# Optimization experiments

Measured on AMD Instinct MI355X. Metric: run time of the kernel, lower is better.

The kernel has to match this reference:

```python
import jax, jax.numpy as jnp
import numpy as np

N_HEADS = 8
EPS = 1e-5

def _mha(q_in, kv_in, wq, bq, wk, bk, wv, bv, wo, bo, causal):
    B, N, D = q_in.shape
    Dh = D // N_HEADS
    # projections (weights stored [in, out])
    Q = (q_in @ wq + bq).reshape(B, N, N_HEADS, Dh).swapaxes(1, 2)  # [B,H,N,Dh]
    K = (kv_in @ wk + bk).reshape(B, N, N_HEADS, Dh).swapaxes(1, 2)
    V = (kv_in @ wv + bv).reshape(B, N, N_HEADS, Dh).swapaxes(1, 2)
    scores = jnp.einsum('bhqd,bhkd->bhqk', Q, K) / jnp.sqrt(jnp.asarray(Dh, q_in.dtype))
    if causal:
        m = jnp.triu(jnp.ones((N, N), dtype=bool), k=1)
        scores = jnp.where(m, jnp.asarray(-jnp.inf, scores.dtype), scores)
    w = jax.nn.softmax(scores, axis=-1)
    attn = jnp.einsum('bhqk,bhkd->bhqd', w, V).swapaxes(1, 2).reshape(B, N, D)
    return attn @ wo + bo

def _ln(x, g, b):
    mu = jnp.mean(x, axis=-1, keepdims=True)
    var = jnp.var(x, axis=-1, keepdims=True)
    return (x - mu) / jnp.sqrt(var + EPS) * g + b

def setup_inputs() -> dict:
    key = jax.random.key(0)
    D, H, S = 512, 8, 4
    ks = jax.random.split(key, 32)
    def w(k, shape):
        return jax.random.normal(k, shape, dtype=jnp.float32) * 0.02
    inp = {
        'x': jax.random.normal(ks[0], (2, 2048, D), dtype=jnp.float32),
        'encoder_output': jax.random.normal(ks[1], (2, 2048, D), dtype=jnp.float32),
        # masked self-attention params
        'm_wq': w(ks[2], (D, D)), 'm_bq': jnp.zeros((D,), jnp.float32),
        'm_wk': w(ks[3], (D, D)), 'm_bk': jnp.zeros((D,), jnp.float32),
        'm_wv': w(ks[4], (D, D)), 'm_bv': jnp.zeros((D,), jnp.float32),
        'm_wo': w(ks[5], (D, D)), 'm_bo': jnp.zeros((D,), jnp.float32),
        # cross-attention params
        'c_wq': w(ks[6], (D, D)), 'c_bq': jnp.zeros((D,), jnp.float32),
        'c_wk': w(ks[7], (D, D)), 'c_bk': jnp.zeros((D,), jnp.float32),
        'c_wv': w(ks[8], (D, D)), 'c_bv': jnp.zeros((D,), jnp.float32),
        'c_wo': w(ks[9], (D, D)), 'c_bo': jnp.zeros((D,), jnp.float32),
        # layer norms
        'ln1_g': jnp.ones((D,), jnp.float32), 'ln1_b': jnp.zeros((D,), jnp.float32),
        'ln2_g': jnp.ones((D,), jnp.float32), 'ln2_b': jnp.zeros((D,), jnp.float32),
        'ln3_g': jnp.ones((D,), jnp.float32), 'ln3_b': jnp.zeros((D,), jnp.float32),
        # feed-forward (scale=4)
        'ff_w1': w(ks[10], (D, S * D)), 'ff_b1': jnp.zeros((S * D,), jnp.float32),
        'ff_w2': w(ks[11], (S * D, D)), 'ff_b2': jnp.zeros((D,), jnp.float32),
    }
    return inp

def reference(x, encoder_output,
              m_wq, m_bq, m_wk, m_bk, m_wv, m_bv, m_wo, m_bo,
              c_wq, c_bq, c_wk, c_bk, c_wv, c_bv, c_wo, c_bo,
              ln1_g, ln1_b, ln2_g, ln2_b, ln3_g, ln3_b,
              ff_w1, ff_b1, ff_w2, ff_b2):
    x = _mha(x, x, m_wq, m_bq, m_wk, m_bk, m_wv, m_bv, m_wo, m_bo, causal=True) + x
    x = _ln(x, ln1_g, ln1_b)
    x = _mha(x, encoder_output, c_wq, c_bq, c_wk, c_bk, c_wv, c_bv, c_wo, c_bo, causal=False) + x
    x = _ln(x, ln2_g, ln2_b)
    h = jax.nn.gelu(x @ ff_w1 + ff_b1, approximate=False)  # torch nn.GELU default = exact erf
    x = h @ ff_w2 + ff_b2 + x
    x = _ln(x, ln3_g, ln3_b)
    return x
```

## Files before the change

kernel.cpp:

```cpp
#include <hip/hip_runtime.h>
#include <hip/hip_bf16.h>

typedef __attribute__((ext_vector_type(8))) short short8;
typedef __attribute__((ext_vector_type(4))) float floatx4;
typedef unsigned short u16;
typedef unsigned int u32;

#define QSCALE 0.1803368801111244f

__device__ __forceinline__ u16 f2b(float f) {
    union { float f; u32 u; } v; v.f = f;
    u32 r = v.u + 0x7fffu + ((v.u >> 16) & 1u);
    return (u16)(r >> 16);
}

__device__ __forceinline__ float b2f(u16 b) {
    u32 u = ((u32)b) << 16;
    union { u32 u; float f; } v; v.u = u;
    return v.f;
}

__device__ __forceinline__ u32 pk2(float a, float b) {
    __hip_bfloat162 w = __float22bfloat162_rn(make_float2(a, b));
    return *(u32*)&w;
}

__device__ __forceinline__ void gload(const u16* g, u16* l) {
    __builtin_amdgcn_global_load_lds((const __attribute__((address_space(1))) void*)g,
                                     (__attribute__((address_space(3))) void*)l, 16, 0, 0);
}

struct TPent { const float* s; u16* d; int O; int dI; };
struct TP16 { TPent e[16]; };
__global__ __launch_bounds__(256) void transpose_convert16(TP16 p) {
    __shared__ float t[32][33];
    TPent e = p.e[blockIdx.z];
    int o0 = blockIdx.x * 32, i0 = blockIdx.y * 32;
    int tx = threadIdx.x, ty = threadIdx.y;
#pragma unroll
    for (int k = 0; k < 32; k += 8) t[ty + k][tx] = e.s[(size_t)(i0 + ty + k) * e.O + o0 + tx];
    __syncthreads();
#pragma unroll
    for (int k = 0; k < 32; k += 8) e.d[(size_t)(o0 + ty + k) * e.dI + i0 + tx] = f2b(t[tx][ty + k]);
}

__global__ __launch_bounds__(256) void gather_bias(const float* b0, const float* b1, const float* b2,
                                                   const float* b3, const float* b4,
                                                   float* dqkv, float* dkv) {
    int i = blockIdx.x * 256 + threadIdx.x;
    if      (i < 512)  dqkv[i] = b0[i];
    else if (i < 1024) dqkv[i] = b1[i - 512];
    else if (i < 1536) dqkv[i] = b2[i - 1024];
    else if (i < 2048) dkv[i - 1536] = b3[i - 1536];
    else               dkv[i - 1536] = b4[i - 2048];
}

__global__ __launch_bounds__(256) void cvt_bf16_2(const float4* __restrict__ s0, ushort4* __restrict__ d0,
                                                  const float4* __restrict__ s1, ushort4* __restrict__ d1) {
    int i = blockIdx.x * 256 + threadIdx.x;
    float4 v = s0[i];
    ushort4 o; o.x = f2b(v.x); o.y = f2b(v.y); o.z = f2b(v.z); o.w = f2b(v.w);
    d0[i] = o;
    v = s1[i];
    o.x = f2b(v.x); o.y = f2b(v.y); o.z = f2b(v.z); o.w = f2b(v.w);
    d1[i] = o;
}

__global__ __launch_bounds__(256) void gemm64x128(
    const u16* __restrict__ A, int lda,
    const u16* __restrict__ B, int ldb,
    int K,
    const float* __restrict__ bias,
    const float* __restrict__ residual,
    float* __restrict__ out_f, u16* __restrict__ out_b,
    int out_stride, int scale_ncols, int gelu_flag)
{
    __shared__ u16 lA[64 * 64];
    __shared__ u16 lB[128 * 64];
    int tid = threadIdx.x, wave = tid >> 6, lane = tid & 63;
    int g4 = lane >> 4, c16 = lane & 15;
    int swz = (c16 & 7) << 3;
    int bm = blockIdx.x * 64, bn = blockIdx.y * 128;
    int wm = (wave >> 1) * 32, wn = (wave & 1) * 64;
    int srow = tid >> 3, skseg = ((tid & 7) * 8) ^ ((srow & 7) << 3);
    const u16* Ar = A + (size_t)(bm + srow) * lda + skseg;
    const u16* Br = B + (size_t)(bn + srow) * ldb + skseg;
    size_t a32 = (size_t)32 * lda, b32 = (size_t)32 * ldb;

    floatx4 acc[2][4];
#pragma unroll
    for (int i = 0; i < 2; i++)
#pragma unroll
        for (int j = 0; j < 4; j++) acc[i][j] = (floatx4){0.f, 0.f, 0.f, 0.f};

    for (int kt = 0; kt < K; kt += 64) {
        __syncthreads();
        gload(Ar + kt,           lA + wave * 512);
        gload(Ar + kt + a32,     lA + 2048 + wave * 512);
        gload(Br + kt,           lB + wave * 512);
        gload(Br + kt + b32,     lB + 2048 + wave * 512);
        gload(Br + kt + 2 * b32, lB + 4096 + wave * 512);
        gload(Br + kt + 3 * b32, lB + 6144 + wave * 512);
        __syncthreads();
        short8 aF[2][2], bF[2][4];
#pragma unroll
        for (int kk = 0; kk < 2; kk++) {
            int ko = (g4 * 8 + kk * 32) ^ swz;
#pragma unroll
            for (int i = 0; i < 2; i++) aF[kk][i] = *(const short8*)&lA[(wm + i * 16 + c16) * 64 + ko];
#pragma unroll
            for (int j = 0; j < 4; j++) bF[kk][j] = *(const short8*)&lB[(wn + j * 16 + c16) * 64 + ko];
        }
#pragma unroll
        for (int kk = 0; kk < 2; kk++)
#pragma unroll
            for (int i = 0; i < 2; i++)
#pragma unroll
                for (int j = 0; j < 4; j++)
                    acc[i][j] = __builtin_amdgcn_mfma_f32_16x16x32_bf16(aF[kk][i], bF[kk][j], acc[i][j], 0, 0, 0);
    }

#pragma unroll
    for (int i = 0; i < 2; i++) {
        int row0 = bm + wm + i * 16 + g4 * 4;
#pragma unroll
        for (int j = 0; j < 4; j++) {
            int col = bn + wn + j * 16 + c16;
            float bv = bias[col];
#pragma unroll
            for (int r = 0; r < 4; r++) {
                int row = row0 + r;
                float v = acc[i][j][r] + bv;
                if (col < scale_ncols) v *= QSCALE;
                if (gelu_flag) v = 0.5f * v * (1.f + erff(v * 0.70710678118654752f));
                if (residual) v += residual[(size_t)row * out_stride + col];
                if (out_f) out_f[(size_t)row * out_stride + col] = v;
                else       out_b[(size_t)row * out_stride + col] = f2b(v);
            }
        }
    }
}

__global__ __launch_bounds__(256) void gemm64x128_dual(
    const u16* __restrict__ A0, const u16* __restrict__ B0, const float* __restrict__ bias0,
    u16* __restrict__ out0, int ostride0, int scale0,
    const u16* __restrict__ A1, const u16* __restrict__ B1, const float* __restrict__ bias1,
    u16* __restrict__ out1, int ostride1,
    int ys, int K, int lda, int ldb)
{
    __shared__ u16 lA[64 * 64];
    __shared__ u16 lB[128 * 64];
    int tid = threadIdx.x, wave = tid >> 6, lane = tid & 63;
    int g4 = lane >> 4, c16 = lane & 15;
    int swz = (c16 & 7) << 3;
    int by = blockIdx.y;
    const u16* A; const u16* B; const float* bias; u16* out; int ostride, scaleN, bn;
    if (by < ys) { A = A0; B = B0; bias = bias0; out = out0; ostride = ostride0; scaleN = scale0; bn = by * 128; }
    else         { A = A1; B = B1; bias = bias1; out = out1; ostride = ostride1; scaleN = 0;      bn = (by - ys) * 128; }
    int bm = blockIdx.x * 64;
    int wm = (wave >> 1) * 32, wn = (wave & 1) * 64;
    int srow = tid >> 3, skseg = ((tid & 7) * 8) ^ ((srow & 7) << 3);
    const u16* Ar = A + (size_t)(bm + srow) * lda + skseg;
    const u16* Br = B + (size_t)(bn + srow) * ldb + skseg;
    size_t a32 = (size_t)32 * lda, b32 = (size_t)32 * ldb;

    floatx4 acc[2][4];
#pragma unroll
    for (int i = 0; i < 2; i++)
#pragma unroll
        for (int j = 0; j < 4; j++) acc[i][j] = (floatx4){0.f, 0.f, 0.f, 0.f};

    for (int kt = 0; kt < K; kt += 64) {
        __syncthreads();
        gload(Ar + kt,           lA + wave * 512);
        gload(Ar + kt + a32,     lA + 2048 + wave * 512);
        gload(Br + kt,           lB + wave * 512);
        gload(Br + kt + b32,     lB + 2048 + wave * 512);
        gload(Br + kt + 2 * b32, lB + 4096 + wave * 512);
        gload(Br + kt + 3 * b32, lB + 6144 + wave * 512);
        __syncthreads();
        short8 aF[2][2], bF[2][4];
#pragma unroll
        for (int kk = 0; kk < 2; kk++) {
            int ko = (g4 * 8 + kk * 32) ^ swz;
#pragma unroll
            for (int i = 0; i < 2; i++) aF[kk][i] = *(const short8*)&lA[(wm + i * 16 + c16) * 64 + ko];
#pragma unroll
            for (int j = 0; j < 4; j++) bF[kk][j] = *(const short8*)&lB[(wn + j * 16 + c16) * 64 + ko];
        }
#pragma unroll
        for (int kk = 0; kk < 2; kk++)
#pragma unroll
            for (int i = 0; i < 2; i++)
#pragma unroll
                for (int j = 0; j < 4; j++)
                    acc[i][j] = __builtin_amdgcn_mfma_f32_16x16x32_bf16(aF[kk][i], bF[kk][j], acc[i][j], 0, 0, 0);
    }

#pragma unroll
    for (int i = 0; i < 2; i++) {
        int row0 = bm + wm + i * 16 + g4 * 4;
#pragma unroll
        for (int j = 0; j < 4; j++) {
            int col = bn + wn + j * 16 + c16;
            float bv = bias[col];
#pragma unroll
            for (int r = 0; r < 4; r++) {
                float v = acc[i][j][r] + bv;
                if (col < scaleN) v *= QSCALE;
                out[(size_t)(row0 + r) * ostride + col] = f2b(v);
            }
        }
    }
}

__global__ __launch_bounds__(256) void gemm64x64(
    const u16* __restrict__ A, int lda,
    const u16* __restrict__ B, int ldb,
    int K,
    const float* __restrict__ bias,
    u16* __restrict__ out_b,
    int out_stride, int scale_ncols)
{
    __shared__ u16 lA[64 * 64];
    __shared__ u16 lB[64 * 64];
    int tid = threadIdx.x, wave = tid >> 6, lane = tid & 63;
    int g4 = lane >> 4, c16 = lane & 15;
    int swz = (c16 & 7) << 3;
    int bm = blockIdx.x * 64, bn = blockIdx.y * 64;
    int wm = wave * 16;
    int srow = tid >> 3, skseg = ((tid & 7) * 8) ^ ((srow & 7) << 3);
    const u16* Ar = A + (size_t)(bm + srow) * lda + skseg;
    const u16* Br = B + (size_t)(bn + srow) * ldb + skseg;
    size_t a32 = (size_t)32 * lda, b32 = (size_t)32 * ldb;

    floatx4 acc[4];
#pragma unroll
    for (int j = 0; j < 4; j++) acc[j] = (floatx4){0.f, 0.f, 0.f, 0.f};

    for (int kt = 0; kt < K; kt += 64) {
        __syncthreads();
        gload(Ar + kt,       lA + wave * 512);
        gload(Ar + kt + a32, lA + 2048 + wave * 512);
        gload(Br + kt,       lB + wave * 512);
        gload(Br + kt + b32, lB + 2048 + wave * 512);
        __syncthreads();
        short8 aF[2], bF[2][4];
#pragma unroll
        for (int kk = 0; kk < 2; kk++) {
            int ko = (g4 * 8 + kk * 32) ^ swz;
            aF[kk] = *(const short8*)&lA[(wm + c16) * 64 + ko];
#pragma unroll
            for (int j = 0; j < 4; j++) bF[kk][j] = *(const short8*)&lB[(j * 16 + c16) * 64 + ko];
        }
#pragma unroll
        for (int kk = 0; kk < 2; kk++)
#pragma unroll
            for (int j = 0; j < 4; j++)
                acc[j] = __builtin_amdgcn_mfma_f32_16x16x32_bf16(aF[kk], bF[kk][j], acc[j], 0, 0, 0);
    }

    int row0 = bm + wm + g4 * 4;
#pragma unroll
    for (int j = 0; j < 4; j++) {
        int col = bn + j * 16 + c16;
        float bv = bias[col];
#pragma unroll
        for (int r = 0; r < 4; r++) {
            int row = row0 + r;
            float v = acc[j][r] + bv;
            if (col < scale_ncols) v *= QSCALE;
            out_b[(size_t)row * out_stride + col] = f2b(v);
        }
    }
}

__global__ __launch_bounds__(256) void gemm64x64s(
    const u16* __restrict__ A, int lda,
    const u16* __restrict__ B, int ldb,
    int Ksub,
    const float* __restrict__ bias,
    const float* __restrict__ res_f,
    const u16* __restrict__ res_b,
    u16* __restrict__ out0, int out_stride)
{
    __shared__ u16 lA[64 * 64];
    __shared__ u16 lB[64 * 64];
    int tid = threadIdx.x, wave = tid >> 6, lane = tid & 63;
    int g4 = lane >> 4, c16 = lane & 15;
    int swz = (c16 & 7) << 3;
    int bm = blockIdx.x * 64, bn = blockIdx.y * 64, sp = blockIdx.z;
    int wm = wave * 16;
    int srow = tid >> 3;
    int skseg = (((tid & 7) * 8) ^ ((srow & 7) << 3)) + sp * Ksub;
    const u16* Ar = A + (size_t)(bm + srow) * lda + skseg;
    const u16* Br = B + (size_t)(bn + srow) * ldb + skseg;
    size_t a32 = (size_t)32 * lda, b32 = (size_t)32 * ldb;

    floatx4 acc[4];
#pragma unroll
    for (int j = 0; j < 4; j++) acc[j] = (floatx4){0.f, 0.f, 0.f, 0.f};

    for (int kt = 0; kt < Ksub; kt += 64) {
        __syncthreads();
        gload(Ar + kt,       lA + wave * 512);
        gload(Ar + kt + a32, lA + 2048 + wave * 512);
        gload(Br + kt,       lB + wave * 512);
        gload(Br + kt + b32, lB + 2048 + wave * 512);
        __syncthreads();
        short8 aF[2], bF[2][4];
#pragma unroll
        for (int kk = 0; kk < 2; kk++) {
            int ko = (g4 * 8 + kk * 32) ^ swz;
            aF[kk] = *(const short8*)&lA[(wm + c16) * 64 + ko];
#pragma unroll
            for (int j = 0; j < 4; j++) bF[kk][j] = *(const short8*)&lB[(j * 16 + c16) * 64 + ko];
        }
#pragma unroll
        for (int kk = 0; kk < 2; kk++)
#pragma unroll
            for (int j = 0; j < 4; j++)
                acc[j] = __builtin_amdgcn_mfma_f32_16x16x32_bf16(aF[kk], bF[kk][j], acc[j], 0, 0, 0);
    }

    u16* out = out0 + (size_t)sp * 4096 * 512;
    int row0 = bm + wm + g4 * 4;
#pragma unroll
    for (int j = 0; j < 4; j++) {
        int col = bn + j * 16 + c16;
        float bv = (sp == 0) ? bias[col] : 0.f;
#pragma unroll
        for (int r = 0; r < 4; r++) {
            int row = row0 + r;
            float v = acc[j][r] + bv;
            if (sp == 0) {
                if (res_f)      v += res_f[(size_t)row * out_stride + col];
                else if (res_b) v += b2f(res_b[(size_t)row * out_stride + col]);
            }
            out[(size_t)row * out_stride + col] = f2b(v);
        }
    }
}

__global__ __launch_bounds__(256, 4) void attn_causal_paired(
    const u16* __restrict__ Qp, int q_stride,
    const u16* __restrict__ Kp, int kv_stride,
    const u16* __restrict__ Vp,
    u16* __restrict__ Opart,
    float* __restrict__ Lpart)
{
    __shared__ u16 lK[64 * 72];
    __shared__ u16 lVT[64 * 72];
    int tid = threadIdx.x, wave = tid >> 6, lane = tid & 63;
    int g4 = lane >> 4, c16 = lane & 15;
    int id = blockIdx.x;
    int bh = (id & 7) | ((id >> 3 & 1) << 3);
    int rest = id >> 4;
    int p = rest & 15;
    int sp = rest >> 4;
    int qtA = p, qtB = 31 - p;
    size_t rowbase = (size_t)(bh >> 3) * 2048;
    int hoff = (bh & 7) * 64;
    const u16* Q = Qp + rowbase * q_stride + hoff;
    const u16* K = Kp + rowbase * kv_stride + hoff;
    const u16* V = Vp + rowbase * kv_stride + hoff;

    int qrowA = qtA * 64 + wave * 16;
    int qrowB = qtB * 64 + wave * 16;
    short8 qa0 = *(const short8*)&Q[(size_t)(qrowA + c16) * q_stride + g4 * 8];
    short8 qa1 = *(const short8*)&Q[(size_t)(qrowA + c16) * q_stride + g4 * 8 + 32];
    short8 qb0 = *(const short8*)&Q[(size_t)(qrowB + c16) * q_stride + g4 * 8];
    short8 qb1 = *(const short8*)&Q[(size_t)(qrowB + c16) * q_stride + g4 * 8 + 32];

    int kr = tid >> 2, ks = (tid & 3) * 16;
    int krow = 16 * (2 * (kr >> 5) + ((kr >> 2) & 1)) + 4 * ((kr >> 3) & 3) + (kr & 3);
    const u16* Kbase = K + (size_t)kr * kv_stride + ks;
    int vk0 = (tid >> 3) * 2, vs = (tid & 7) * 8;
    const u16* Vbase = V + (size_t)vk0 * kv_stride + vs;

    int4 kv0, kv1, vv0, vv1;
    auto load_tile = [&](int kt) {
        const u16* kp = Kbase + (size_t)kt * 64 * kv_stride;
        kv0 = *(const int4*)(kp);
        kv1 = *(const int4*)(kp + 8);
        const u16* vp = Vbase + (size_t)kt * 64 * kv_stride;
        vv0 = *(const int4*)(vp);
        vv1 = *(const int4*)(vp + kv_stride);
    };
    auto store_tile = [&]() {
        *(int4*)&lK[krow * 72 + ks] = kv0;
        *(int4*)&lK[krow * 72 + ks + 8] = kv1;
        const u16* pa = (const u16*)&vv0;
        const u16* pb = (const u16*)&vv1;
#pragma unroll
        for (int j = 0; j < 8; j++) {
            int dh = vs + j;
            int keyS = vk0 ^ (((dh >> 3) & 3) << 4);
            u32 w = (u32)pa[j] | ((u32)pb[j] << 16);
            *(u32*)&lVT[dh * 72 + keyS] = w;
        }
    };

    floatx4 oA[4], oB[4];
#pragma unroll
    for (int d = 0; d < 4; d++) { oA[d] = (floatx4){0.f,0.f,0.f,0.f}; oB[d] = (floatx4){0.f,0.f,0.f,0.f}; }
    float lsA = 0.f, lsB = 0.f;

    auto compute_tile = [&](short8 qf0, short8 qf1, floatx4 (&oacc)[4], float& lsum,
                            bool diag, int qtile, int kt) {
        floatx4 sc[4];
#pragma unroll
        for (int nt = 0; nt < 4; nt++) {
            short8 b0 = *(const short8*)&lK[(nt * 16 + c16) * 72 + g4 * 8];
            short8 b1 = *(const short8*)&lK[(nt * 16 + c16) * 72 + g4 * 8 + 32];
            floatx4 z = (floatx4){0.f, 0.f, 0.f, 0.f};
            z = __builtin_amdgcn_mfma_f32_16x16x32_bf16(b0, qf0, z, 0, 0, 0);
            z = __builtin_amdgcn_mfma_f32_16x16x32_bf16(b1, qf1, z, 0, 0, 0);
            sc[nt] = z;
        }
        if (diag) {
            int qr = qtile * 64 + wave * 16 + c16;
#pragma unroll
            for (int nt = 0; nt < 4; nt++) {
                int key0 = kt * 64 + 8 * g4 + 4 * (nt & 1) + 32 * (nt >> 1);
#pragma unroll
                for (int r = 0; r < 4; r++)
                    if (key0 + r > qr) sc[nt][r] = -1e30f;
            }
        }
        float e[4][4];
#pragma unroll
        for (int nt = 0; nt < 4; nt++)
#pragma unroll
            for (int r = 0; r < 4; r++) e[nt][r] = exp2f(sc[nt][r]);
        float s0 = (e[0][0] + e[0][1]) + (e[0][2] + e[0][3]);
        float s1 = (e[1][0] + e[1][1]) + (e[1][2] + e[1][3]);
        float s2 = (e[2][0] + e[2][1]) + (e[2][2] + e[2][3]);
        float s3 = (e[3][0] + e[3][1]) + (e[3][2] + e[3][3]);
        lsum += (s0 + s1) + (s2 + s3);
        short8 pa0, pa1;
        {
            u32 w[8];
            w[0] = pk2(e[0][0], e[0][1]); w[1] = pk2(e[0][2], e[0][3]);
            w[2] = pk2(e[1][0], e[1][1]); w[3] = pk2(e[1][2], e[1][3]);
            w[4] = pk2(e[2][0], e[2][1]); w[5] = pk2(e[2][2], e[2][3]);
            w[6] = pk2(e[3][0], e[3][1]); w[7] = pk2(e[3][2], e[3][3]);
            pa0 = *(short8*)&w[0];
            pa1 = *(short8*)&w[4];
        }
#pragma unroll
        for (int d = 0; d < 4; d++) {
            int vswz = ((2 * d + (c16 >> 3)) & 3) << 4;
            short8 vb0 = *(const short8*)&lVT[(d * 16 + c16) * 72 + ((g4 * 8) ^ vswz)];
            short8 vb1 = *(const short8*)&lVT[(d * 16 + c16) * 72 + ((32 + g4 * 8) ^ vswz)];
            oacc[d] = __builtin_amdgcn_mfma_f32_16x16x32_bf16(pa0, vb0, oacc[d], 0, 0, 0);
            oacc[d] = __builtin_amdgcn_mfma_f32_16x16x32_bf16(pa1, vb1, oacc[d], 0, 0, 0);
        }
    };

    int t = sp;
    load_tile(t <= p ? t : t - p - 1);
    for (; t < 33; t += 4) {
        __syncthreads();
        store_tile();
        __syncthreads();
        if (t + 4 < 33) { int tn = t + 4; load_tile(tn <= p ? tn : tn - p - 1); }
        if (t <= p) compute_tile(qa0, qa1, oA, lsA, t == p,  qtA, t);
        else        compute_tile(qb0, qb1, oB, lsB, t == 32, qtB, t - p - 1);
    }

    lsA += __shfl_xor(lsA, 16); lsA += __shfl_xor(lsA, 32);
    lsB += __shfl_xor(lsB, 16); lsB += __shfl_xor(lsB, 32);
    size_t slab = (size_t)(sp * 16 + bh) * 2048;
    if (g4 == 0) {
        Lpart[slab + qrowA + c16] = lsA;
        Lpart[slab + qrowB + c16] = lsB;
    }
    u16* ObA = Opart + (slab + qrowA) * 64;
    u16* ObB = Opart + (slab + qrowB) * 64;
#pragma unroll
    for (int d = 0; d < 4; d++)
#pragma unroll
        for (int r = 0; r < 4; r++) {
            ObA[(size_t)(4 * g4 + r) * 64 + d * 16 + c16] = f2b(oA[d][r]);
            ObB[(size_t)(4 * g4 + r) * 64 + d * 16 + c16] = f2b(oB[d][r]);
        }
}

__global__ __launch_bounds__(256) void attn_fused(
    const u16* __restrict__ Qp, int q_stride,
    const u16* __restrict__ Kp, int kv_stride,
    const u16* __restrict__ Vp,
    u16* __restrict__ Opart,
    float* __restrict__ Lpart)
{
    __shared__ u16 lK[64 * 72];
    __shared__ u16 lVT[64 * 72];
    int tid = threadIdx.x, wave = tid >> 6, lane = tid & 63;
    int g4 = lane >> 4, c16 = lane & 15;
    int id = blockIdx.x;
    int bh = (id & 7) | ((id >> 3 & 1) << 3);
    int rest = id >> 4;
    int qt = rest & 31;
    int sp = rest >> 5;
    size_t rowbase = (size_t)(bh >> 3) * 2048;
    int hoff = (bh & 7) * 64;
    const u16* Q = Qp + rowbase * q_stride + hoff;
    const u16* K = Kp + rowbase * kv_stride + hoff;
    const u16* V = Vp + rowbase * kv_stride + hoff;

    int qrow0 = qt * 64 + wave * 16;
    short8 qf0 = *(const short8*)&Q[(size_t)(qrow0 + c16) * q_stride + g4 * 8];
    short8 qf1 = *(const short8*)&Q[(size_t)(qrow0 + c16) * q_stride + g4 * 8 + 32];

    int kr = tid >> 2, ks = (tid & 3) * 16;
    int krow = 16 * (2 * (kr >> 5) + ((kr >> 2) & 1)) + 4 * ((kr >> 3) & 3) + (kr & 3);
    const u16* Kbase = K + (size_t)kr * kv_stride + ks;
    int vk0 = (tid >> 3) * 2, vs = (tid & 7) * 8;
    const u16* Vbase = V + (size_t)vk0 * kv_stride + vs;

    int4 kv0, kv1, vv0, vv1;
    auto load_tile = [&](int kt) {
        const u16* kp = Kbase + (size_t)kt * 64 * kv_stride;
        kv0 = *(const int4*)(kp);
        kv1 = *(const int4*)(kp + 8);
        const u16* vp = Vbase + (size_t)kt * 64 * kv_stride;
        vv0 = *(const int4*)(vp);
        vv1 = *(const int4*)(vp + kv_stride);
    };
    auto store_tile = [&]() {
        *(int4*)&lK[krow * 72 + ks] = kv0;
        *(int4*)&lK[krow * 72 + ks + 8] = kv1;
        const u16* pa = (const u16*)&vv0;
        const u16* pb = (const u16*)&vv1;
#pragma unroll
        for (int j = 0; j < 8; j++) {
            int dh = vs + j;
            int keyS = vk0 ^ (((dh >> 3) & 3) << 4);
            u32 w = (u32)pa[j] | ((u32)pb[j] << 16);
            *(u32*)&lVT[dh * 72 + keyS] = w;
        }
    };

    floatx4 o_acc[4];
#pragma unroll
    for (int d = 0; d < 4; d++) o_acc[d] = (floatx4){0.f, 0.f, 0.f, 0.f};
    float lsum = 0.f;

    int kt = sp;
    load_tile(kt);
    for (; kt < 32; kt += 4) {
        __syncthreads();
        store_tile();
        __syncthreads();
        if (kt + 4 < 32) load_tile(kt + 4);

        floatx4 sc[4];
#pragma unroll
        for (int nt = 0; nt < 4; nt++) {
            short8 b0 = *(const short8*)&lK[(nt * 16 + c16) * 72 + g4 * 8];
            short8 b1 = *(const short8*)&lK[(nt * 16 + c16) * 72 + g4 * 8 + 32];
            floatx4 z = (floatx4){0.f, 0.f, 0.f, 0.f};
            z = __builtin_amdgcn_mfma_f32_16x16x32_bf16(b0, qf0, z, 0, 0, 0);
            z = __builtin_amdgcn_mfma_f32_16x16x32_bf16(b1, qf1, z, 0, 0, 0);
            sc[nt] = z;
        }
        float e[4][4];
#pragma unroll
        for (int nt = 0; nt < 4; nt++)
#pragma unroll
            for (int r = 0; r < 4; r++) e[nt][r] = exp2f(sc[nt][r]);
        float s0 = (e[0][0] + e[0][1]) + (e[0][2] + e[0][3]);
        float s1 = (e[1][0] + e[1][1]) + (e[1][2] + e[1][3]);
        float s2 = (e[2][0] + e[2][1]) + (e[2][2] + e[2][3]);
        float s3 = (e[3][0] + e[3][1]) + (e[3][2] + e[3][3]);
        lsum += (s0 + s1) + (s2 + s3);
        short8 pa0, pa1;
        {
            u32 w[8];
            w[0] = pk2(e[0][0], e[0][1]); w[1] = pk2(e[0][2], e[0][3]);
            w[2] = pk2(e[1][0], e[1][1]); w[3] = pk2(e[1][2], e[1][3]);
            w[4] = pk2(e[2][0], e[2][1]); w[5] = pk2(e[2][2], e[2][3]);
            w[6] = pk2(e[3][0], e[3][1]); w[7] = pk2(e[3][2], e[3][3]);
            pa0 = *(short8*)&w[0];
            pa1 = *(short8*)&w[4];
        }
#pragma unroll
        for (int d = 0; d < 4; d++) {
            int swz = ((2 * d + (c16 >> 3)) & 3) << 4;
            short8 vb0 = *(const short8*)&lVT[(d * 16 + c16) * 72 + ((g4 * 8) ^ swz)];
            short8 vb1 = *(const short8*)&lVT[(d * 16 + c16) * 72 + ((32 + g4 * 8) ^ swz)];
            o_acc[d] = __builtin_amdgcn_mfma_f32_16x16x32_bf16(pa0, vb0, o_acc[d], 0, 0, 0);
            o_acc[d] = __builtin_amdgcn_mfma_f32_16x16x32_bf16(pa1, vb1, o_acc[d], 0, 0, 0);
        }
    }

    lsum += __shfl_xor(lsum, 16);
    lsum += __shfl_xor(lsum, 32);
    size_t slab = (size_t)(sp * 16 + bh) * 2048;
    if (g4 == 0) Lpart[slab + qrow0 + c16] = lsum;
    u16* Ob = Opart + (slab + qrow0) * 64;
#pragma unroll
    for (int d = 0; d < 4; d++)
#pragma unroll
        for (int r = 0; r < 4; r++)
            Ob[(size_t)(4 * g4 + r) * 64 + d * 16 + c16] = f2b(o_acc[d][r]);
}

__global__ __launch_bounds__(256) void attn_combine(
    const ushort4* __restrict__ Op,
    const float* __restrict__ Lp,
    ushort4* __restrict__ out)
{
    int e = blockIdx.x * 256 + threadIdx.x;
    int dh4 = e & 15;
    int qrow = (e >> 4) & 2047;
    int bh = e >> 15;
    int li = bh * 2048 + qrow;
    float l = (Lp[li] + Lp[32768 + li]) + (Lp[65536 + li] + Lp[98304 + li]);
    float inv = 1.f / l;
    ushort4 a = Op[e];
    ushort4 b = Op[524288 + e];
    ushort4 c = Op[2 * 524288 + e];
    ushort4 d = Op[3 * 524288 + e];
    ushort4 o;
    o.x = f2b(((b2f(a.x) + b2f(b.x)) + (b2f(c.x) + b2f(d.x))) * inv);
    o.y = f2b(((b2f(a.y) + b2f(b.y)) + (b2f(c.y) + b2f(d.y))) * inv);
    o.z = f2b(((b2f(a.z) + b2f(b.z)) + (b2f(c.z) + b2f(d.z))) * inv);
    o.w = f2b(((b2f(a.w) + b2f(b.w)) + (b2f(c.w) + b2f(d.w))) * inv);
    int row = (bh >> 3) * 2048 + qrow;
    out[(size_t)row * 128 + (bh & 7) * 16 + dh4] = o;
}

__global__ __launch_bounds__(256) void ln_kernel(const u16* __restrict__ in0,
                                                 const u16* __restrict__ in1,
                                                 const float* __restrict__ g,
                                                 const float* __restrict__ b,
                                                 float* __restrict__ out_f,
                                                 u16* __restrict__ out_b)
{
    const int D = 512;
    int row = blockIdx.x, tid = threadIdx.x;
    size_t base = (size_t)row * D;
    float v0 = b2f(in0[base + tid]) + b2f(in1[base + tid]);
    float v1 = b2f(in0[base + tid + 256]) + b2f(in1[base + tid + 256]);
    float s = v0 + v1, ss = v0 * v0 + v1 * v1;
#pragma unroll
    for (int off = 1; off < 64; off <<= 1) { s += __shfl_xor(s, off); ss += __shfl_xor(ss, off); }
    __shared__ float red[8];
    int wave = tid >> 6, lane = tid & 63;
    if (lane == 0) { red[wave] = s; red[4 + wave] = ss; }
    __syncthreads();
    float st = red[0] + red[1] + red[2] + red[3];
    float sst = red[4] + red[5] + red[6] + red[7];
    float mu = st * (1.f / 512.f);
    float var = sst * (1.f / 512.f) - mu * mu;
    float rs = rsqrtf(var + 1e-5f);
    float y0 = (v0 - mu) * rs * g[tid] + b[tid];
    float y1 = (v1 - mu) * rs * g[tid + 256] + b[tid + 256];
    if (out_f) { out_f[base + tid] = y0; out_f[base + tid + 256] = y1; }
    if (out_b) { out_b[base + tid] = f2b(y0); out_b[base + tid + 256] = f2b(y1); }
}

extern "C" void kernel_launch(void* const* d_in, const int* in_sizes, int n_in,
                              void* d_out, int out_size, void* d_ws, size_t ws_size,
                              hipStream_t stream)
{
    (void)in_sizes; (void)n_in; (void)out_size; (void)ws_size;
    const float* x     = (const float*)d_in[0];
    const float* enc   = (const float*)d_in[1];
    const float* m_wq  = (const float*)d_in[2];  const float* m_bq = (const float*)d_in[3];
    const float* m_wk  = (const float*)d_in[4];  const float* m_bk = (const float*)d_in[5];
    const float* m_wv  = (const float*)d_in[6];  const float* m_bv = (const float*)d_in[7];
    const float* m_wo  = (const float*)d_in[8];  const float* m_bo = (const float*)d_in[9];
    const float* c_wq  = (const float*)d_in[10]; const float* c_bq = (const float*)d_in[11];
    const float* c_wk  = (const float*)d_in[12]; const float* c_bk = (const float*)d_in[13];
    const float* c_wv  = (const float*)d_in[14]; const float* c_bv = (const float*)d_in[15];
    const float* c_wo  = (const float*)d_in[16]; const float* c_bo = (const float*)d_in[17];
    const float* ln1_g = (const float*)d_in[18]; const float* ln1_b = (const float*)d_in[19];
    const float* ln2_g = (const float*)d_in[20]; const float* ln2_b = (const float*)d_in[21];
    const float* ln3_g = (const float*)d_in[22]; const float* ln3_b = (const float*)d_in[23];
    const float* ff_w1 = (const float*)d_in[24]; const float* ff_b1 = (const float*)d_in[25];
    const float* ff_w2 = (const float*)d_in[26]; const float* ff_b2 = (const float*)d_in[27];

    char* base = (char*)d_ws; size_t off = 0;
    auto alloc = [&](size_t bytes) -> void* {
        void* p = base + off; off = (off + bytes + 255) & ~(size_t)255; return p;
    };
    u16*   Wqkv_m = (u16*)alloc(1536 * 512 * 2);
    u16*   Wo_m   = (u16*)alloc(512 * 512 * 2);
    u16*   Wq_c   = (u16*)alloc(512 * 512 * 2);
    u16*   Wkv_c  = (u16*)alloc(1024 * 512 * 2);
    u16*   Wo_c   = (u16*)alloc(512 * 512 * 2);
    u16*   W1t    = (u16*)alloc(2048 * 512 * 2);
    u16*   W2t    = (u16*)alloc(512 * 2048 * 2);
    float* bqkv_m = (float*)alloc(1536 * 4);
    float* bkv_c  = (float*)alloc(1024 * 4);
    u16*   xb     = (u16*)alloc((size_t)4096 * 512 * 2);
    u16*   encb   = (u16*)alloc((size_t)4096 * 512 * 2);
    u16*   qkvm   = (u16*)alloc((size_t)4096 * 1536 * 2);
    u16*   attnm  = (u16*)alloc((size_t)4096 * 512 * 2);
    u16*   y01    = (u16*)alloc((size_t)2 * 4096 * 512 * 2);
    u16*   x1b    = (u16*)alloc((size_t)4096 * 512 * 2);
    u16*   qc     = (u16*)alloc((size_t)4096 * 512 * 2);
    u16*   kvc    = (u16*)alloc((size_t)4096 * 1024 * 2);
    u16*   attnc  = (u16*)alloc((size_t)4096 * 512 * 2);
    u16*   x2b    = (u16*)alloc((size_t)4096 * 512 * 2);
    u16*   h      = (u16*)alloc((size_t)4096 * 2048 * 2);
    u16*   Opart  = (u16*)alloc((size_t)4 * 16 * 2048 * 64 * 2);
    float* Lpart  = (float*)alloc((size_t)4 * 16 * 2048 * 4);

    TP16 tp;
    tp.e[0] = {m_wq, Wqkv_m,              512, 512};
    tp.e[1] = {m_wk, Wqkv_m + 512 * 512,  512, 512};
    tp.e[2] = {m_wv, Wqkv_m + 1024 * 512, 512, 512};
    tp.e[3] = {m_wo, Wo_m,                512, 512};
    tp.e[4] = {c_wq, Wq_c,                512, 512};
    tp.e[5] = {c_wk, Wkv_c,               512, 512};
    tp.e[6] = {c_wv, Wkv_c + 512 * 512,   512, 512};
    tp.e[7] = {c_wo, Wo_c,                512, 512};
    for (int k = 0; k < 4; k++)
        tp.e[8 + k]  = {ff_w1 + 512 * k,        W1t + k * 512 * 512, 2048, 512};
    for (int k = 0; k < 4; k++)
        tp.e[12 + k] = {ff_w2 + (size_t)512 * k * 512, W2t + 512 * k, 512, 2048};
    transpose_convert16<<<dim3(16, 16, 16), dim3(32, 8), 0, stream>>>(tp);
    gather_bias<<<10, 256, 0, stream>>>(m_bq, m_bk, m_bv, c_bk, c_bv, bqkv_m, bkv_c);
    cvt_bf16_2<<<2048, 256, 0, stream>>>((const float4*)x, (ushort4*)xb,
                                         (const float4*)enc, (ushort4*)encb);

    gemm64x128_dual<<<dim3(64, 20), 256, 0, stream>>>(
        xb, Wqkv_m, bqkv_m, qkvm, 1536, 512,
        encb, Wkv_c, bkv_c, kvc, 1024,
        12, 512, 512, 512);

    attn_causal_paired<<<1024, 256, 0, stream>>>(qkvm, 1536, qkvm + 512, 1536, qkvm + 1024,
                                                 Opart, Lpart);
    attn_combine<<<2048, 256, 0, stream>>>((const ushort4*)Opart, Lpart, (ushort4*)attnm);
    gemm64x64s<<<dim3(64, 8, 2), 256, 0, stream>>>(attnm, 512, Wo_m, 512, 256,
                                                   m_bo, x, nullptr, y01, 512);
    ln_kernel<<<4096, 256, 0, stream>>>(y01, y01 + (size_t)4096 * 512, ln1_g, ln1_b,
                                        nullptr, x1b);

    gemm64x64<<<dim3(64, 8), 256, 0, stream>>>(x1b, 512, Wq_c, 512, 512,
                                               c_bq, qc, 512, 512);
    attn_fused<<<2048, 256, 0, stream>>>(qc, 512, kvc, 1024, kvc + 512,
                                         Opart, Lpart);
    attn_combine<<<2048, 256, 0, stream>>>((const ushort4*)Opart, Lpart, (ushort4*)attnc);
    gemm64x64s<<<dim3(64, 8, 2), 256, 0, stream>>>(attnc, 512, Wo_c, 512, 256,
                                                   c_bo, nullptr, x1b, y01, 512);
    ln_kernel<<<4096, 256, 0, stream>>>(y01, y01 + (size_t)4096 * 512, ln2_g, ln2_b,
                                        nullptr, x2b);

    gemm64x128<<<dim3(64, 16), 256, 0, stream>>>(x2b, 512, W1t, 512, 512,
                                                 ff_b1, nullptr, nullptr, h, 2048, 0, 1);
    gemm64x64s<<<dim3(64, 8, 2), 256, 0, stream>>>(h, 2048, W2t, 2048, 1024,
                                                   ff_b2, nullptr, x2b, y01, 512);
    ln_kernel<<<4096, 256, 0, stream>>>(y01, y01 + (size_t)4096 * 512, ln3_g, ln3_b,
                                        (float*)d_out, nullptr);
}
```

Before: 308.0 us.

## Use 128-row query tiles per block in causal and cross attention

Both attention kernels now give each wave 32 query rows (two 16-row MFMA chunks) instead of 16. Every K/V tile staged in LDS therefore feeds twice as many query rows, and the grids shrink to 512 and 1024 blocks. The causal kernel keeps its paired light/heavy scheduling, rescaled to 128-row tiles over 34 key steps split four ways, with masking applied on the diagonal tiles. The cost is more registers per thread (occupancy hints lowered to 2 and 3 blocks) and fewer blocks to spread across the CUs.

```diff
diff --git a/kernel.cpp b/kernel.cpp
--- a/kernel.cpp
+++ b/kernel.cpp
@@ -342,7 +342,8 @@
     }
 }
 
-__global__ __launch_bounds__(256, 4) void attn_causal_paired(
+
+__global__ __launch_bounds__(256, 3) void attn_cross(
     const u16* __restrict__ Qp, int q_stride,
     const u16* __restrict__ Kp, int kv_stride,
     const u16* __restrict__ Vp,
@@ -356,21 +357,21 @@
     int id = blockIdx.x;
     int bh = (id & 7) | ((id >> 3 & 1) << 3);
     int rest = id >> 4;
-    int p = rest & 15;
+    int qt = rest & 15;
     int sp = rest >> 4;
-    int qtA = p, qtB = 31 - p;
     size_t rowbase = (size_t)(bh >> 3) * 2048;
     int hoff = (bh & 7) * 64;
     const u16* Q = Qp + rowbase * q_stride + hoff;
     const u16* K = Kp + rowbase * kv_stride + hoff;
     const u16* V = Vp + rowbase * kv_stride + hoff;
 
-    int qrowA = qtA * 64 + wave * 16;
-    int qrowB = qtB * 64 + wave * 16;
-    short8 qa0 = *(const short8*)&Q[(size_t)(qrowA + c16) * q_stride + g4 * 8];
-    short8 qa1 = *(const short8*)&Q[(size_t)(qrowA + c16) * q_stride + g4 * 8 + 32];
-    short8 qb0 = *(const short8*)&Q[(size_t)(qrowB + c16) * q_stride + g4 * 8];
-    short8 qb1 = *(const short8*)&Q[(size_t)(qrowB + c16) * q_stride + g4 * 8 + 32];
+    int qbase = qt * 128 + wave * 32;
+    short8 qf[2][2];
+#pragma unroll
+    for (int qc = 0; qc < 2; qc++) {
+        qf[qc][0] = *(const short8*)&Q[(size_t)(qbase + qc * 16 + c16) * q_stride + g4 * 8];
+        qf[qc][1] = *(const short8*)&Q[(size_t)(qbase + qc * 16 + c16) * q_stride + g4 * 8 + 32];
+    }
 
     int kr = tid >> 2, ks = (tid & 3) * 16;
     int krow = 16 * (2 * (kr >> 5) + ((kr >> 2) & 1)) + 4 * ((kr >> 3) & 3) + (kr & 3);
@@ -401,93 +402,88 @@
         }
     };
 
-    floatx4 oA[4], oB[4];
-#pragma unroll
-    for (int d = 0; d < 4; d++) { oA[d] = (floatx4){0.f,0.f,0.f,0.f}; oB[d] = (floatx4){0.f,0.f,0.f,0.f}; }
-    float lsA = 0.f, lsB = 0.f;
-
-    auto compute_tile = [&](short8 qf0, short8 qf1, floatx4 (&oacc)[4], float& lsum,
-                            bool diag, int qtile, int kt) {
-        floatx4 sc[4];
+    floatx4 o[2][4];
+#pragma unroll
+    for (int qc = 0; qc < 2; qc++)
+#pragma unroll
+        for (int d = 0; d < 4; d++) o[qc][d] = (floatx4){0.f, 0.f, 0.f, 0.f};
+    float ls0 = 0.f, ls1 = 0.f;
+
+    int kt = sp;
+    load_tile(kt);
+    for (; kt < 32; kt += 4) {
+        __syncthreads();
+        store_tile();
+        __syncthreads();
+        if (kt + 4 < 32) load_tile(kt + 4);
+
+        short8 b0[4], b1[4];
 #pragma unroll
         for (int nt = 0; nt < 4; nt++) {
-            short8 b0 = *(const short8*)&lK[(nt * 16 + c16) * 72 + g4 * 8];
-            short8 b1 = *(const short8*)&lK[(nt * 16 + c16) * 72 + g4 * 8 + 32];
-            floatx4 z = (floatx4){0.f, 0.f, 0.f, 0.f};
-            z = __builtin_amdgcn_mfma_f32_16x16x32_bf16(b0, qf0, z, 0, 0, 0);
-            z = __builtin_amdgcn_mfma_f32_16x16x32_bf16(b1, qf1, z, 0, 0, 0);
-            sc[nt] = z;
-        }
-        if (diag) {
-            int qr = qtile * 64 + wave * 16 + c16;
+            b0[nt] = *(const short8*)&lK[(nt * 16 + c16) * 72 + g4 * 8];
+            b1[nt] = *(const short8*)&lK[(nt * 16 + c16) * 72 + g4 * 8 + 32];
+        }
+        short8 pa[2][2];
+#pragma unroll
+        for (int qc = 0; qc < 2; qc++) {
+            floatx4 sc[4];
 #pragma unroll
             for (int nt = 0; nt < 4; nt++) {
-                int key0 = kt * 64 + 8 * g4 + 4 * (nt & 1) + 32 * (nt >> 1);
-#pragma unroll
-                for (int r = 0; r < 4; r++)
-                    if (key0 + r > qr) sc[nt][r] = -1e30f;
+                floatx4 z = (floatx4){0.f, 0.f, 0.f, 0.f};
+                z = __builtin_amdgcn_mfma_f32_16x16x32_bf16(b0[nt], qf[qc][0], z, 0, 0, 0);
+                z = __builtin_amdgcn_mfma_f32_16x16x32_bf16(b1[nt], qf[qc][1], z, 0, 0, 0);
+                sc[nt] = z;
             }
-        }
-        float e[4][4];
-#pragma unroll
-        for (int nt = 0; nt < 4; nt++)
-#pragma unroll
-            for (int r = 0; r < 4; r++) e[nt][r] = exp2f(sc[nt][r]);
-        float s0 = (e[0][0] + e[0][1]) + (e[0][2] + e[0][3]);
-        float s1 = (e[1][0] + e[1][1]) + (e[1][2] + e[1][3]);
-        float s2 = (e[2][0] + e[2][1]) + (e[2][2] + e[2][3]);
-        float s3 = (e[3][0] + e[3][1]) + (e[3][2] + e[3][3]);
-        lsum += (s0 + s1) + (s2 + s3);
-        short8 pa0, pa1;
-        {
+            float e[4][4];
+#pragma unroll
+            for (int nt = 0; nt < 4; nt++)
+#pragma unroll
+                for (int r = 0; r < 4; r++) e[nt][r] = exp2f(sc[nt][r]);
+            float s0 = (e[0][0] + e[0][1]) + (e[0][2] + e[0][3]);
+            float s1 = (e[1][0] + e[1][1]) + (e[1][2] + e[1][3]);
+            float s2 = (e[2][0] + e[2][1]) + (e[2][2] + e[2][3]);
+            float s3 = (e[3][0] + e[3][1]) + (e[3][2] + e[3][3]);
+            if (qc == 0) ls0 += (s0 + s1) + (s2 + s3);
+            else         ls1 += (s0 + s1) + (s2 + s3);
             u32 w[8];
             w[0] = pk2(e[0][0], e[0][1]); w[1] = pk2(e[0][2], e[0][3]);
             w[2] = pk2(e[1][0], e[1][1]); w[3] = pk2(e[1][2], e[1][3]);
             w[4] = pk2(e[2][0], e[2][1]); w[5] = pk2(e[2][2], e[2][3]);
             w[6] = pk2(e[3][0], e[3][1]); w[7] = pk2(e[3][2], e[3][3]);
-            pa0 = *(short8*)&w[0];
-            pa1 = *(short8*)&w[4];
+            pa[qc][0] = *(short8*)&w[0];
+            pa[qc][1] = *(short8*)&w[4];
         }
 #pragma unroll
         for (int d = 0; d < 4; d++) {
             int vswz = ((2 * d + (c16 >> 3)) & 3) << 4;
             short8 vb0 = *(const short8*)&lVT[(d * 16 + c16) * 72 + ((g4 * 8) ^ vswz)];
             short8 vb1 = *(const short8*)&lVT[(d * 16 + c16) * 72 + ((32 + g4 * 8) ^ vswz)];
-            oacc[d] = __builtin_amdgcn_mfma_f32_16x16x32_bf16(pa0, vb0, oacc[d], 0, 0, 0);
-            oacc[d] = __builtin_amdgcn_mfma_f32_16x16x32_bf16(pa1, vb1, oacc[d], 0, 0, 0);
-        }
-    };
-
-    int t = sp;
-    load_tile(t <= p ? t : t - p - 1);
-    for (; t < 33; t += 4) {
-        __syncthreads();
-        store_tile();
-        __syncthreads();
-        if (t + 4 < 33) { int tn = t + 4; load_tile(tn <= p ? tn : tn - p - 1); }
-        if (t <= p) compute_tile(qa0, qa1, oA, lsA, t == p,  qtA, t);
-        else        compute_tile(qb0, qb1, oB, lsB, t == 32, qtB, t - p - 1);
-    }
-
-    lsA += __shfl_xor(lsA, 16); lsA += __shfl_xor(lsA, 32);
-    lsB += __shfl_xor(lsB, 16); lsB += __shfl_xor(lsB, 32);
+            o[0][d] = __builtin_amdgcn_mfma_f32_16x16x32_bf16(pa[0][0], vb0, o[0][d], 0, 0, 0);
+            o[0][d] = __builtin_amdgcn_mfma_f32_16x16x32_bf16(pa[0][1], vb1, o[0][d], 0, 0, 0);
+            o[1][d] = __builtin_amdgcn_mfma_f32_16x16x32_bf16(pa[1][0], vb0, o[1][d], 0, 0, 0);
+            o[1][d] = __builtin_amdgcn_mfma_f32_16x16x32_bf16(pa[1][1], vb1, o[1][d], 0, 0, 0);
+        }
+    }
+
+    ls0 += __shfl_xor(ls0, 16); ls0 += __shfl_xor(ls0, 32);
+    ls1 += __shfl_xor(ls1, 16); ls1 += __shfl_xor(ls1, 32);
     size_t slab = (size_t)(sp * 16 + bh) * 2048;
     if (g4 == 0) {
-        Lpart[slab + qrowA + c16] = lsA;
-        Lpart[slab + qrowB + c16] = lsB;
-    }
-    u16* ObA = Opart + (slab + qrowA) * 64;
-    u16* ObB = Opart + (slab + qrowB) * 64;
-#pragma unroll
-    for (int d = 0; d < 4; d++)
-#pragma unroll
-        for (int r = 0; r < 4; r++) {
-            ObA[(size_t)(4 * g4 + r) * 64 + d * 16 + c16] = f2b(oA[d][r]);
-            ObB[(size_t)(4 * g4 + r) * 64 + d * 16 + c16] = f2b(oB[d][r]);
-        }
-}
-
-__global__ __launch_bounds__(256) void attn_fused(
+        Lpart[slab + qbase + c16] = ls0;
+        Lpart[slab + qbase + 16 + c16] = ls1;
+    }
+#pragma unroll
+    for (int qc = 0; qc < 2; qc++) {
+        u16* Ob = Opart + (slab + qbase + qc * 16) * 64;
+#pragma unroll
+        for (int d = 0; d < 4; d++)
+#pragma unroll
+            for (int r = 0; r < 4; r++)
+                Ob[(size_t)(4 * g4 + r) * 64 + d * 16 + c16] = f2b(o[qc][d][r]);
+    }
+}
+
+__global__ __launch_bounds__(256, 2) void attn_causal_paired(
     const u16* __restrict__ Qp, int q_stride,
     const u16* __restrict__ Kp, int kv_stride,
     const u16* __restrict__ Vp,
@@ -501,17 +497,26 @@
     int id = blockIdx.x;
     int bh = (id & 7) | ((id >> 3 & 1) << 3);
     int rest = id >> 4;
-    int qt = rest & 31;
-    int sp = rest >> 5;
+    int p = rest & 7;
+    int sp = rest >> 3;
+    int TqA = p, TqB = 15 - p;
+    int splitA = 2 * p + 2;
     size_t rowbase = (size_t)(bh >> 3) * 2048;
     int hoff = (bh & 7) * 64;
     const u16* Q = Qp + rowbase * q_stride + hoff;
     const u16* K = Kp + rowbase * kv_stride + hoff;
     const u16* V = Vp + rowbase * kv_stride + hoff;
 
-    int qrow0 = qt * 64 + wave * 16;
-    short8 qf0 = *(const short8*)&Q[(size_t)(qrow0 + c16) * q_stride + g4 * 8];
-    short8 qf1 = *(const short8*)&Q[(size_t)(qrow0 + c16) * q_stride + g4 * 8 + 32];
+    int qbA = TqA * 128 + wave * 32;
+    int qbB = TqB * 128 + wave * 32;
+    short8 qfA[2][2], qfB[2][2];
+#pragma unroll
+    for (int qc = 0; qc < 2; qc++) {
+        qfA[qc][0] = *(const short8*)&Q[(size_t)(qbA + qc * 16 + c16) * q_stride + g4 * 8];
+        qfA[qc][1] = *(const short8*)&Q[(size_t)(qbA + qc * 16 + c16) * q_stride + g4 * 8 + 32];
+        qfB[qc][0] = *(const short8*)&Q[(size_t)(qbB + qc * 16 + c16) * q_stride + g4 * 8];
+        qfB[qc][1] = *(const short8*)&Q[(size_t)(qbB + qc * 16 + c16) * q_stride + g4 * 8 + 32];
+    }
 
     int kr = tid >> 2, ks = (tid & 3) * 16;
     int krow = 16 * (2 * (kr >> 5) + ((kr >> 2) & 1)) + 4 * ((kr >> 3) & 3) + (kr & 3);
@@ -531,80 +536,124 @@
     auto store_tile = [&]() {
         *(int4*)&lK[krow * 72 + ks] = kv0;
         *(int4*)&lK[krow * 72 + ks + 8] = kv1;
-        const u16* pa = (const u16*)&vv0;
-        const u16* pb = (const u16*)&vv1;
+        const u16* pa_ = (const u16*)&vv0;
+        const u16* pb_ = (const u16*)&vv1;
 #pragma unroll
         for (int j = 0; j < 8; j++) {
             int dh = vs + j;
             int keyS = vk0 ^ (((dh >> 3) & 3) << 4);
-            u32 w = (u32)pa[j] | ((u32)pb[j] << 16);
+            u32 w = (u32)pa_[j] | ((u32)pb_[j] << 16);
             *(u32*)&lVT[dh * 72 + keyS] = w;
         }
     };
 
-    floatx4 o_acc[4];
-#pragma unroll
-    for (int d = 0; d < 4; d++) o_acc[d] = (floatx4){0.f, 0.f, 0.f, 0.f};
-    float lsum = 0.f;
-
-    int kt = sp;
-    load_tile(kt);
-    for (; kt < 32; kt += 4) {
-        __syncthreads();
-        store_tile();
-        __syncthreads();
-        if (kt + 4 < 32) load_tile(kt + 4);
-
-        floatx4 sc[4];
+    floatx4 oA[2][4], oB[2][4];
+#pragma unroll
+    for (int qc = 0; qc < 2; qc++)
+#pragma unroll
+        for (int d = 0; d < 4; d++) {
+            oA[qc][d] = (floatx4){0.f, 0.f, 0.f, 0.f};
+            oB[qc][d] = (floatx4){0.f, 0.f, 0.f, 0.f};
+        }
+    float lsA0 = 0.f, lsA1 = 0.f, lsB0 = 0.f, lsB1 = 0.f;
+
+    auto compute_tile = [&](short8 (&qf)[2][2], floatx4 (&oacc)[2][4], float& l0, float& l1,
+                            int qb, int kt, bool dg) {
+        short8 b0[4], b1[4];
 #pragma unroll
         for (int nt = 0; nt < 4; nt++) {
-            short8 b0 = *(const short8*)&lK[(nt * 16 + c16) * 72 + g4 * 8];
-            short8 b1 = *(const short8*)&lK[(nt * 16 + c16) * 72 + g4 * 8 + 32];
-            floatx4 z = (floatx4){0.f, 0.f, 0.f, 0.f};
-            z = __builtin_amdgcn_mfma_f32_16x16x32_bf16(b0, qf0, z, 0, 0, 0);
-            z = __builtin_amdgcn_mfma_f32_16x16x32_bf16(b1, qf1, z, 0, 0, 0);
-            sc[nt] = z;
-        }
-        float e[4][4];
-#pragma unroll
-        for (int nt = 0; nt < 4; nt++)
-#pragma unroll
-            for (int r = 0; r < 4; r++) e[nt][r] = exp2f(sc[nt][r]);
-        float s0 = (e[0][0] + e[0][1]) + (e[0][2] + e[0][3]);
-        float s1 = (e[1][0] + e[1][1]) + (e[1][2] + e[1][3]);
-        float s2 = (e[2][0] + e[2][1]) + (e[2][2] + e[2][3]);
-        float s3 = (e[3][0] + e[3][1]) + (e[3][2] + e[3][3]);
-        lsum += (s0 + s1) + (s2 + s3);
-        short8 pa0, pa1;
-        {
+            b0[nt] = *(const short8*)&lK[(nt * 16 + c16) * 72 + g4 * 8];
+            b1[nt] = *(const short8*)&lK[(nt * 16 + c16) * 72 + g4 * 8 + 32];
+        }
+        short8 pa[2][2];
+#pragma unroll
+        for (int qc = 0; qc < 2; qc++) {
+            floatx4 sc[4];
+#pragma unroll
+            for (int nt = 0; nt < 4; nt++) {
+                floatx4 z = (floatx4){0.f, 0.f, 0.f, 0.f};
+                z = __builtin_amdgcn_mfma_f32_16x16x32_bf16(b0[nt], qf[qc][0], z, 0, 0, 0);
+                z = __builtin_amdgcn_mfma_f32_16x16x32_bf16(b1[nt], qf[qc][1], z, 0, 0, 0);
+                sc[nt] = z;
+            }
+            if (dg) {
+                int qr = qb + qc * 16 + c16;
+#pragma unroll
+                for (int nt = 0; nt < 4; nt++) {
+                    int key0 = kt * 64 + 8 * g4 + 4 * (nt & 1) + 32 * (nt >> 1);
+#pragma unroll
+                    for (int r = 0; r < 4; r++)
+                        if (key0 + r > qr) sc[nt][r] = -1e30f;
+                }
+            }
+            float e[4][4];
+#pragma unroll
+            for (int nt = 0; nt < 4; nt++)
+#pragma unroll
+                for (int r = 0; r < 4; r++) e[nt][r] = exp2f(sc[nt][r]);
+            float s0 = (e[0][0] + e[0][1]) + (e[0][2] + e[0][3]);
+            float s1 = (e[1][0] + e[1][1]) + (e[1][2] + e[1][3]);
+            float s2 = (e[2][0] + e[2][1]) + (e[2][2] + e[2][3]);
+            float s3 = (e[3][0] + e[3][1]) + (e[3][2] + e[3][3]);
+            if (qc == 0) l0 += (s0 + s1) + (s2 + s3);
+            else         l1 += (s0 + s1) + (s2 + s3);
             u32 w[8];
             w[0] = pk2(e[0][0], e[0][1]); w[1] = pk2(e[0][2], e[0][3]);
             w[2] = pk2(e[1][0], e[1][1]); w[3] = pk2(e[1][2], e[1][3]);
             w[4] = pk2(e[2][0], e[2][1]); w[5] = pk2(e[2][2], e[2][3]);
             w[6] = pk2(e[3][0], e[3][1]); w[7] = pk2(e[3][2], e[3][3]);
-            pa0 = *(short8*)&w[0];
-            pa1 = *(short8*)&w[4];
+            pa[qc][0] = *(short8*)&w[0];
+            pa[qc][1] = *(short8*)&w[4];
         }
 #pragma unroll
         for (int d = 0; d < 4; d++) {
-            int swz = ((2 * d + (c16 >> 3)) & 3) << 4;
-            short8 vb0 = *(const short8*)&lVT[(d * 16 + c16) * 72 + ((g4 * 8) ^ swz)];
-            short8 vb1 = *(const short8*)&lVT[(d * 16 + c16) * 72 + ((32 + g4 * 8) ^ swz)];
-            o_acc[d] = __builtin_amdgcn_mfma_f32_16x16x32_bf16(pa0, vb0, o_acc[d], 0, 0, 0);
-            o_acc[d] = __builtin_amdgcn_mfma_f32_16x16x32_bf16(pa1, vb1, o_acc[d], 0, 0, 0);
-        }
-    }
-
-    lsum += __shfl_xor(lsum, 16);
-    lsum += __shfl_xor(lsum, 32);
+            int vswz = ((2 * d + (c16 >> 3)) & 3) << 4;
+            short8 vb0 = *(const short8*)&lVT[(d * 16 + c16) * 72 + ((g4 * 8) ^ vswz)];
+            short8 vb1 = *(const short8*)&lVT[(d * 16 + c16) * 72 + ((32 + g4 * 8) ^ vswz)];
+            oacc[0][d] = __builtin_amdgcn_mfma_f32_16x16x32_bf16(pa[0][0], vb0, oacc[0][d], 0, 0, 0);
+            oacc[0][d] = __builtin_amdgcn_mfma_f32_16x16x32_bf16(pa[0][1], vb1, oacc[0][d], 0, 0, 0);
+            oacc[1][d] = __builtin_amdgcn_mfma_f32_16x16x32_bf16(pa[1][0], vb0, oacc[1][d], 0, 0, 0);
+            oacc[1][d] = __builtin_amdgcn_mfma_f32_16x16x32_bf16(pa[1][1], vb1, oacc[1][d], 0, 0, 0);
+        }
+    };
+
+    int t = sp;
+    load_tile(t < splitA ? t : t - splitA);
+    for (; t < 34; t += 4) {
+        __syncthreads();
+        store_tile();
+        __syncthreads();
+        if (t + 4 < 34) { int tn = t + 4; load_tile(tn < splitA ? tn : tn - splitA); }
+        if (t < splitA) compute_tile(qfA, oA, lsA0, lsA1, qbA, t, t >= 2 * TqA);
+        else {
+            int kt = t - splitA;
+            compute_tile(qfB, oB, lsB0, lsB1, qbB, kt, kt >= 2 * TqB);
+        }
+    }
+
+    lsA0 += __shfl_xor(lsA0, 16); lsA0 += __shfl_xor(lsA0, 32);
+    lsA1 += __shfl_xor(lsA1, 16); lsA1 += __shfl_xor(lsA1, 32);
+    lsB0 += __shfl_xor(lsB0, 16); lsB0 += __shfl_xor(lsB0, 32);
+    lsB1 += __shfl_xor(lsB1, 16); lsB1 += __shfl_xor(lsB1, 32);
     size_t slab = (size_t)(sp * 16 + bh) * 2048;
-    if (g4 == 0) Lpart[slab + qrow0 + c16] = lsum;
-    u16* Ob = Opart + (slab + qrow0) * 64;
-#pragma unroll
-    for (int d = 0; d < 4; d++)
-#pragma unroll
-        for (int r = 0; r < 4; r++)
-            Ob[(size_t)(4 * g4 + r) * 64 + d * 16 + c16] = f2b(o_acc[d][r]);
+    if (g4 == 0) {
+        Lpart[slab + qbA + c16] = lsA0;
+        Lpart[slab + qbA + 16 + c16] = lsA1;
+        Lpart[slab + qbB + c16] = lsB0;
+        Lpart[slab + qbB + 16 + c16] = lsB1;
+    }
+#pragma unroll
+    for (int qc = 0; qc < 2; qc++) {
+        u16* ObA = Opart + (slab + qbA + qc * 16) * 64;
+        u16* ObB = Opart + (slab + qbB + qc * 16) * 64;
+#pragma unroll
+        for (int d = 0; d < 4; d++)
+#pragma unroll
+            for (int r = 0; r < 4; r++) {
+                ObA[(size_t)(4 * g4 + r) * 64 + d * 16 + c16] = f2b(oA[qc][d][r]);
+                ObB[(size_t)(4 * g4 + r) * 64 + d * 16 + c16] = f2b(oB[qc][d][r]);
+            }
+    }
 }
 
 __global__ __launch_bounds__(256) void attn_combine(
@@ -733,8 +782,8 @@
         encb, Wkv_c, bkv_c, kvc, 1024,
         12, 512, 512, 512);
 
-    attn_causal_paired<<<1024, 256, 0, stream>>>(qkvm, 1536, qkvm + 512, 1536, qkvm + 1024,
-                                                 Opart, Lpart);
+    attn_causal_paired<<<512, 256, 0, stream>>>(qkvm, 1536, qkvm + 512, 1536, qkvm + 1024,
+                                                Opart, Lpart);
     attn_combine<<<2048, 256, 0, stream>>>((const ushort4*)Opart, Lpart, (ushort4*)attnm);
     gemm64x64s<<<dim3(64, 8, 2), 256, 0, stream>>>(attnm, 512, Wo_m, 512, 256,
                                                    m_bo, x, nullptr, y01, 512);
@@ -743,7 +792,7 @@
 
     gemm64x64<<<dim3(64, 8), 256, 0, stream>>>(x1b, 512, Wq_c, 512, 512,
                                                c_bq, qc, 512, 512);
-    attn_fused<<<2048, 256, 0, stream>>>(qc, 512, kvc, 1024, kvc + 512,
+    attn_cross<<<1024, 256, 0, stream>>>(qc, 512, kvc, 1024, kvc + 512,
                                          Opart, Lpart);
     attn_combine<<<2048, 256, 0, stream>>>((const ushort4*)Opart, Lpart, (ushort4*)attnc);
     gemm64x64s<<<dim3(64, 8, 2), 256, 0, stream>>>(attnc, 512, Wo_c, 512, 256,
```

Result: faster. 293.4 us (-4.7%).
